# Kernel tuning notes

Measured on AMD Instinct MI355X. Metric: run time of the kernel, lower is better.

Reference implementation:

```python
import jax, jax.numpy as jnp
import numpy as np


def setup_inputs() -> dict:
    key = jax.random.key(0)
    k1, k2 = jax.random.split(key)
    src = jax.random.normal(k1, (16, 3, 1024, 1024), dtype=jnp.float32)
    dst = jax.random.normal(k2, (16, 3, 1024, 1024), dtype=jnp.float32)
    return {"src": src, "dst": dst}


def reference(src, dst):
    b, c, h, w = src.shape  # c == 3
    A = src.reshape(b, c, h * w)  # (b, 3, N)
    B = dst.reshape(b, c, h * w)
    Amean = jnp.mean(A, axis=-1, keepdims=True)  # (b, 3, 1)
    Bmean = jnp.mean(B, axis=-1, keepdims=True)
    Ac = A - Amean
    Bc = B - Bmean
    # covariance-like 3x3 matrices over the large spatial dim
    AAt = jnp.einsum('bin,bjn->bij', Ac, Ac)  # (b, 3, 3)
    BAt = jnp.einsum('bin,bjn->bij', Bc, Ac)
    AAt = AAt + 0.001 * jnp.eye(c, dtype=AAt.dtype)
    AAti = jnp.linalg.inv(AAt)
    x = jnp.einsum('bij,bjk->bik', BAt, AAti)  # (b, 3, 3)
    C = jnp.einsum('bij,bjn->bin', x, Ac) + Bmean  # (b, 3, N)
    return C.reshape(b, c, h, w)
```

## Files before the change

### kernel.cpp

```cpp
#include <hip/hip_runtime.h>

#define NPIX  (1024 * 1024)
#define NVEC  (NPIX / 4)
#define NSTAT 21
#define RBLOCKS  128
#define RTHREADS 256
#define RITERS (NVEC / (RBLOCKS * RTHREADS))
#define RSTRIDE (RBLOCKS * RTHREADS)

__global__ __launch_bounds__(RTHREADS, 2) void reduce_stats(
    const float4* __restrict__ src, const float4* __restrict__ dst,
    double* __restrict__ partials)
{
    const int b  = blockIdx.y;
    const int pb = blockIdx.x;

    const float4* A0 = src + (size_t)b * 3 * NVEC;
    const float4* A1 = A0 + NVEC;
    const float4* A2 = A0 + 2 * NVEC;
    const float4* B0 = dst + (size_t)b * 3 * NVEC;
    const float4* B1 = B0 + NVEC;
    const float4* B2 = B0 + 2 * NVEC;

    float acc[NSTAT];
#pragma unroll
    for (int s = 0; s < NSTAT; ++s) acc[s] = 0.0f;

#define ACC1(A0v, A1v, A2v, B0v, B1v, B2v)                                   \
    do {                                                                     \
        acc[0] += (A0v); acc[1] += (A1v); acc[2] += (A2v);                   \
        acc[3] += (B0v); acc[4] += (B1v); acc[5] += (B2v);                   \
        acc[6]  = fmaf((A0v), (A0v), acc[6]);                                \
        acc[7]  = fmaf((A0v), (A1v), acc[7]);                                \
        acc[8]  = fmaf((A0v), (A2v), acc[8]);                                \
        acc[9]  = fmaf((A1v), (A1v), acc[9]);                                \
        acc[10] = fmaf((A1v), (A2v), acc[10]);                               \
        acc[11] = fmaf((A2v), (A2v), acc[11]);                               \
        acc[12] = fmaf((B0v), (A0v), acc[12]);                               \
        acc[13] = fmaf((B0v), (A1v), acc[13]);                               \
        acc[14] = fmaf((B0v), (A2v), acc[14]);                               \
        acc[15] = fmaf((B1v), (A0v), acc[15]);                               \
        acc[16] = fmaf((B1v), (A1v), acc[16]);                               \
        acc[17] = fmaf((B1v), (A2v), acc[17]);                               \
        acc[18] = fmaf((B2v), (A0v), acc[18]);                               \
        acc[19] = fmaf((B2v), (A1v), acc[19]);                               \
        acc[20] = fmaf((B2v), (A2v), acc[20]);                               \
    } while (0)

#define GLD(dstv, p) \
    asm volatile("global_load_dwordx4 %0, %1, off" : "=v"(dstv) : "v"(p) : "memory")

#define ISSUE(s, k)                                                          \
    do {                                                                     \
        const int pp = p0 + (k) * RSTRIDE;                                   \
        GLD(s##0, A0 + pp); GLD(s##1, A1 + pp); GLD(s##2, A2 + pp);          \
        GLD(s##3, B0 + pp); GLD(s##4, B1 + pp); GLD(s##5, B2 + pp);          \
    } while (0)

#define WAIT6() do {                                                         \
        asm volatile("s_waitcnt vmcnt(6)" ::: "memory");                     \
        __builtin_amdgcn_sched_barrier(0); } while (0)
#define WAIT0() do {                                                         \
        asm volatile("s_waitcnt vmcnt(0)" ::: "memory");                     \
        __builtin_amdgcn_sched_barrier(0); } while (0)

#define ACCS(s)                                                              \
    do {                                                                     \
        ACC1((s##0).x, (s##1).x, (s##2).x, (s##3).x, (s##4).x, (s##5).x);    \
        ACC1((s##0).y, (s##1).y, (s##2).y, (s##3).y, (s##4).y, (s##5).y);    \
        ACC1((s##0).z, (s##1).z, (s##2).z, (s##3).z, (s##4).z, (s##5).z);    \
        ACC1((s##0).w, (s##1).w, (s##2).w, (s##3).w, (s##4).w, (s##5).w);    \
    } while (0)

    const int p0 = pb * RTHREADS + threadIdx.x;

    float4 x0, x1, x2, x3, x4, x5;
    float4 y0, y1, y2, y3, y4, y5;
    float4 z0, z1, z2, z3, z4, z5;

    ISSUE(x, 0);
    ISSUE(y, 1);
    WAIT6(); ISSUE(z, 2); ACCS(x);
    WAIT6(); ISSUE(x, 3); ACCS(y);
    WAIT6(); ISSUE(y, 4); ACCS(z);
    WAIT6(); ISSUE(z, 5); ACCS(x);
    WAIT6(); ISSUE(x, 6); ACCS(y);
    WAIT6(); ISSUE(y, 7); ACCS(z);
    WAIT6();              ACCS(x);
    WAIT0();              ACCS(y);
#undef ISSUE
#undef GLD
#undef WAIT6
#undef WAIT0
#undef ACCS
#undef ACC1

    double accd[NSTAT];
#pragma unroll
    for (int s = 0; s < NSTAT; ++s) {
        double v = (double)acc[s];
        for (int off = 32; off > 0; off >>= 1) v += __shfl_down(v, off, 64);
        accd[s] = v;
    }

    __shared__ double part[RTHREADS / 64][NSTAT];
    const int lane = threadIdx.x & 63;
    const int wid  = threadIdx.x >> 6;
    if (lane == 0) {
#pragma unroll
        for (int s = 0; s < NSTAT; ++s) part[wid][s] = accd[s];
    }
    __syncthreads();

    if (threadIdx.x < NSTAT) {
        const int s = threadIdx.x;
        double v = part[0][s] + part[1][s] + part[2][s] + part[3][s];
        partials[((size_t)b * NSTAT + s) * RBLOCKS + pb] = v;
    }
}

__global__ __launch_bounds__(RBLOCKS) void solve3x3(
    const double* __restrict__ partials, float* __restrict__ coef)
{
    const int b = blockIdx.x;
    const int t = threadIdx.x;

    __shared__ double wsum[NSTAT][2];

#pragma unroll
    for (int s = 0; s < NSTAT; ++s) {
        double v = partials[((size_t)b * NSTAT + s) * RBLOCKS + t];
        for (int off = 32; off > 0; off >>= 1) v += __shfl_down(v, off, 64);
        if ((t & 63) == 0) wsum[s][t >> 6] = v;
    }
    __syncthreads();

    if (t == 0) {
        double st[NSTAT];
#pragma unroll
        for (int s = 0; s < NSTAT; ++s) st[s] = wsum[s][0] + wsum[s][1];

        const double N = (double)NPIX;
        double am[3] = {st[0] / N, st[1] / N, st[2] / N};
        double bm[3] = {st[3] / N, st[4] / N, st[5] / N};

        double AA[3][3];
        AA[0][0] = st[6]  - N * am[0] * am[0] + 0.001;
        AA[0][1] = st[7]  - N * am[0] * am[1];
        AA[0][2] = st[8]  - N * am[0] * am[2];
        AA[1][1] = st[9]  - N * am[1] * am[1] + 0.001;
        AA[1][2] = st[10] - N * am[1] * am[2];
        AA[2][2] = st[11] - N * am[2] * am[2] + 0.001;
        AA[1][0] = AA[0][1]; AA[2][0] = AA[0][2]; AA[2][1] = AA[1][2];

        double BA[3][3];
#pragma unroll
        for (int i = 0; i < 3; ++i)
#pragma unroll
            for (int j = 0; j < 3; ++j)
                BA[i][j] = st[12 + 3 * i + j] - N * bm[i] * am[j];

        double c00 =  AA[1][1] * AA[2][2] - AA[1][2] * AA[2][1];
        double c01 = -(AA[1][0] * AA[2][2] - AA[1][2] * AA[2][0]);
        double c02 =  AA[1][0] * AA[2][1] - AA[1][1] * AA[2][0];
        double det = AA[0][0] * c00 + AA[0][1] * c01 + AA[0][2] * c02;
        double id  = 1.0 / det;

        double inv[3][3];
        inv[0][0] = c00 * id;
        inv[1][0] = c01 * id;
        inv[2][0] = c02 * id;
        inv[0][1] = -(AA[0][1] * AA[2][2] - AA[0][2] * AA[2][1]) * id;
        inv[1][1] =  (AA[0][0] * AA[2][2] - AA[0][2] * AA[2][0]) * id;
        inv[2][1] = -(AA[0][0] * AA[2][1] - AA[0][1] * AA[2][0]) * id;
        inv[0][2] =  (AA[0][1] * AA[1][2] - AA[0][2] * AA[1][1]) * id;
        inv[1][2] = -(AA[0][0] * AA[1][2] - AA[0][2] * AA[1][0]) * id;
        inv[2][2] =  (AA[0][0] * AA[1][1] - AA[0][1] * AA[1][0]) * id;

        double X[3][3];
#pragma unroll
        for (int i = 0; i < 3; ++i)
#pragma unroll
            for (int j = 0; j < 3; ++j)
                X[i][j] = BA[i][0] * inv[0][j] + BA[i][1] * inv[1][j] +
                          BA[i][2] * inv[2][j];

        float* cb = coef + b * 12;
#pragma unroll
        for (int i = 0; i < 3; ++i) {
#pragma unroll
            for (int j = 0; j < 3; ++j) cb[3 * i + j] = (float)X[i][j];
            cb[9 + i] = (float)(bm[i] - (X[i][0] * am[0] + X[i][1] * am[1] +
                                         X[i][2] * am[2]));
        }
    }
}

__global__ __launch_bounds__(256, 2) void apply_map(
    const float4* __restrict__ src, float4* __restrict__ out,
    const float* __restrict__ coef)
{
    const int b = blockIdx.y;
    const float* cb = coef + b * 12;
    const float x00 = cb[0], x01 = cb[1], x02 = cb[2];
    const float x10 = cb[3], x11 = cb[4], x12 = cb[5];
    const float x20 = cb[6], x21 = cb[7], x22 = cb[8];
    const float o0 = cb[9], o1 = cb[10], o2 = cb[11];

    const float4* A0 = src + (size_t)b * 3 * NVEC;
    const float4* A1 = A0 + NVEC;
    const float4* A2 = A0 + 2 * NVEC;
    float4* O0 = out + (size_t)b * 3 * NVEC;
    float4* O1 = O0 + NVEC;
    float4* O2 = O0 + 2 * NVEC;

    const int p0 = blockIdx.x * 256 + threadIdx.x;

#define ALOAD(s, k)                                                          \
    do {                                                                     \
        const int pp = p0 + (k) * RSTRIDE;                                   \
        s##0 = A0[pp]; s##1 = A1[pp]; s##2 = A2[pp];                         \
    } while (0)

#define ASTORE(s, k)                                                         \
    do {                                                                     \
        const int pp = p0 + (k) * RSTRIDE;                                   \
        float4 r0, r1, r2;                                                   \
        r0.x = fmaf(x00, (s##0).x, fmaf(x01, (s##1).x, fmaf(x02, (s##2).x, o0))); \
        r1.x = fmaf(x10, (s##0).x, fmaf(x11, (s##1).x, fmaf(x12, (s##2).x, o1))); \
        r2.x = fmaf(x20, (s##0).x, fmaf(x21, (s##1).x, fmaf(x22, (s##2).x, o2))); \
        r0.y = fmaf(x00, (s##0).y, fmaf(x01, (s##1).y, fmaf(x02, (s##2).y, o0))); \
        r1.y = fmaf(x10, (s##0).y, fmaf(x11, (s##1).y, fmaf(x12, (s##2).y, o1))); \
        r2.y = fmaf(x20, (s##0).y, fmaf(x21, (s##1).y, fmaf(x22, (s##2).y, o2))); \
        r0.z = fmaf(x00, (s##0).z, fmaf(x01, (s##1).z, fmaf(x02, (s##2).z, o0))); \
        r1.z = fmaf(x10, (s##0).z, fmaf(x11, (s##1).z, fmaf(x12, (s##2).z, o1))); \
        r2.z = fmaf(x20, (s##0).z, fmaf(x21, (s##1).z, fmaf(x22, (s##2).z, o2))); \
        r0.w = fmaf(x00, (s##0).w, fmaf(x01, (s##1).w, fmaf(x02, (s##2).w, o0))); \
        r1.w = fmaf(x10, (s##0).w, fmaf(x11, (s##1).w, fmaf(x12, (s##2).w, o1))); \
        r2.w = fmaf(x20, (s##0).w, fmaf(x21, (s##1).w, fmaf(x22, (s##2).w, o2))); \
        O0[pp] = r0; O1[pp] = r1; O2[pp] = r2;                               \
    } while (0)

    float4 u0, u1, u2;
    float4 v0, v1, v2;
    float4 w0, w1, w2;

    ALOAD(u, 0);
    ALOAD(v, 1);
    ALOAD(w, 2);  ASTORE(u, 0);
    ALOAD(u, 3);  ASTORE(v, 1);
    ALOAD(v, 4);  ASTORE(w, 2);
    ALOAD(w, 5);  ASTORE(u, 3);
    ALOAD(u, 6);  ASTORE(v, 4);
    ALOAD(v, 7);  ASTORE(w, 5);
                  ASTORE(u, 6);
                  ASTORE(v, 7);
#undef ALOAD
#undef ASTORE
}

extern "C" void kernel_launch(void* const* d_in, const int* in_sizes, int n_in,
                              void* d_out, int out_size, void* d_ws, size_t ws_size,
                              hipStream_t stream)
{
    const float4* src = (const float4*)d_in[0];
    const float4* dst = (const float4*)d_in[1];
    float4* out = (float4*)d_out;

    const int batches = in_sizes[0] / (3 * NPIX);

    double* partials = (double*)d_ws;
    float*  coef = (float*)((char*)d_ws +
                            (size_t)batches * NSTAT * RBLOCKS * sizeof(double));

    reduce_stats<<<dim3(RBLOCKS, batches), RTHREADS, 0, stream>>>(src, dst, partials);
    solve3x3<<<batches, RBLOCKS, 0, stream>>>(partials, (float*)coef);
    apply_map<<<dim3(RBLOCKS, batches), 256, 0, stream>>>(src, out, coef);
}
```

Measured before the change: 506.8 us.

## Stage reduction loads through LDS with direct global-to-LDS double buffering

After: 511.8 us. About the same (+1.0%).

```diff
diff --git a/kernel.cpp b/kernel.cpp
--- a/kernel.cpp
+++ b/kernel.cpp
@@ -7,6 +7,14 @@
 #define RTHREADS 256
 #define RITERS (NVEC / (RBLOCKS * RTHREADS))
 #define RSTRIDE (RBLOCKS * RTHREADS)
+#define TILE 256
+
+__device__ __forceinline__ void gld_lds16(const float4* g, float4* l) {
+    __builtin_amdgcn_global_load_lds(
+        (const __attribute__((address_space(1))) void*)(g),
+        (__attribute__((address_space(3))) void*)(l),
+        16, 0, 0);
+}
 
 __global__ __launch_bounds__(RTHREADS, 2) void reduce_stats(
     const float4* __restrict__ src, const float4* __restrict__ dst,
@@ -14,13 +22,18 @@
 {
     const int b  = blockIdx.y;
     const int pb = blockIdx.x;
-
-    const float4* A0 = src + (size_t)b * 3 * NVEC;
-    const float4* A1 = A0 + NVEC;
-    const float4* A2 = A0 + 2 * NVEC;
-    const float4* B0 = dst + (size_t)b * 3 * NVEC;
-    const float4* B1 = B0 + NVEC;
-    const float4* B2 = B0 + 2 * NVEC;
+    const int wv = threadIdx.x >> 6;
+    const int ln = threadIdx.x & 63;
+
+    const float4* P[6];
+    P[0] = src + (size_t)b * 3 * NVEC;
+    P[1] = P[0] + NVEC;
+    P[2] = P[0] + 2 * NVEC;
+    P[3] = dst + (size_t)b * 3 * NVEC;
+    P[4] = P[3] + NVEC;
+    P[5] = P[3] + 2 * NVEC;
+
+    __shared__ float4 stage[2][6][TILE];
 
     float acc[NSTAT];
 #pragma unroll
@@ -47,14 +60,15 @@
         acc[20] = fmaf((B2v), (A2v), acc[20]);                               \
     } while (0)
 
-#define GLD(dstv, p) \
-    asm volatile("global_load_dwordx4 %0, %1, off" : "=v"(dstv) : "v"(p) : "memory")
-
-#define ISSUE(s, k)                                                          \
-    do {                                                                     \
-        const int pp = p0 + (k) * RSTRIDE;                                   \
-        GLD(s##0, A0 + pp); GLD(s##1, A1 + pp); GLD(s##2, A2 + pp);          \
-        GLD(s##3, B0 + pp); GLD(s##4, B1 + pp); GLD(s##5, B2 + pp);          \
+#define STAGE(bufi, k)                                                       \
+    do {                                                                     \
+        const int g = pb * RTHREADS + (k) * RSTRIDE + wv * 64 + ln;          \
+        gld_lds16(P[0] + g, &stage[bufi][0][wv * 64]);                       \
+        gld_lds16(P[1] + g, &stage[bufi][1][wv * 64]);                       \
+        gld_lds16(P[2] + g, &stage[bufi][2][wv * 64]);                       \
+        gld_lds16(P[3] + g, &stage[bufi][3][wv * 64]);                       \
+        gld_lds16(P[4] + g, &stage[bufi][4][wv * 64]);                       \
+        gld_lds16(P[5] + g, &stage[bufi][5][wv * 64]);                       \
     } while (0)
 
 #define WAIT6() do {                                                         \
@@ -63,36 +77,31 @@
 #define WAIT0() do {                                                         \
         asm volatile("s_waitcnt vmcnt(0)" ::: "memory");                     \
         __builtin_amdgcn_sched_barrier(0); } while (0)
-
-#define ACCS(s)                                                              \
-    do {                                                                     \
-        ACC1((s##0).x, (s##1).x, (s##2).x, (s##3).x, (s##4).x, (s##5).x);    \
-        ACC1((s##0).y, (s##1).y, (s##2).y, (s##3).y, (s##4).y, (s##5).y);    \
-        ACC1((s##0).z, (s##1).z, (s##2).z, (s##3).z, (s##4).z, (s##5).z);    \
-        ACC1((s##0).w, (s##1).w, (s##2).w, (s##3).w, (s##4).w, (s##5).w);    \
-    } while (0)
-
-    const int p0 = pb * RTHREADS + threadIdx.x;
-
-    float4 x0, x1, x2, x3, x4, x5;
-    float4 y0, y1, y2, y3, y4, y5;
-    float4 z0, z1, z2, z3, z4, z5;
-
-    ISSUE(x, 0);
-    ISSUE(y, 1);
-    WAIT6(); ISSUE(z, 2); ACCS(x);
-    WAIT6(); ISSUE(x, 3); ACCS(y);
-    WAIT6(); ISSUE(y, 4); ACCS(z);
-    WAIT6(); ISSUE(z, 5); ACCS(x);
-    WAIT6(); ISSUE(x, 6); ACCS(y);
-    WAIT6(); ISSUE(y, 7); ACCS(z);
-    WAIT6();              ACCS(x);
-    WAIT0();              ACCS(y);
-#undef ISSUE
-#undef GLD
+#define BAR() asm volatile("s_barrier" ::: "memory")
+
+    STAGE(0, 0);
+#pragma unroll
+    for (int k = 0; k < RITERS; ++k) {
+        const int cb = k & 1;
+        if (k < RITERS - 1) { STAGE(cb ^ 1, k + 1); WAIT6(); }
+        else                { WAIT0(); }
+        BAR();
+        const float4 a0 = stage[cb][0][threadIdx.x];
+        const float4 a1 = stage[cb][1][threadIdx.x];
+        const float4 a2 = stage[cb][2][threadIdx.x];
+        const float4 b0 = stage[cb][3][threadIdx.x];
+        const float4 b1 = stage[cb][4][threadIdx.x];
+        const float4 b2 = stage[cb][5][threadIdx.x];
+        ACC1(a0.x, a1.x, a2.x, b0.x, b1.x, b2.x);
+        ACC1(a0.y, a1.y, a2.y, b0.y, b1.y, b2.y);
+        ACC1(a0.z, a1.z, a2.z, b0.z, b1.z, b2.z);
+        ACC1(a0.w, a1.w, a2.w, b0.w, b1.w, b2.w);
+        if (k < RITERS - 1) BAR();
+    }
+#undef STAGE
 #undef WAIT6
 #undef WAIT0
-#undef ACCS
+#undef BAR
 #undef ACC1
 
     double accd[NSTAT];
@@ -104,11 +113,9 @@
     }
 
     __shared__ double part[RTHREADS / 64][NSTAT];
-    const int lane = threadIdx.x & 63;
-    const int wid  = threadIdx.x >> 6;
-    if (lane == 0) {
-#pragma unroll
-        for (int s = 0; s < NSTAT; ++s) part[wid][s] = accd[s];
+    if (ln == 0) {
+#pragma unroll
+        for (int s = 0; s < NSTAT; ++s) part[wv][s] = accd[s];
     }
     __syncthreads();
 
```
